# Kernel optimization log

Hardware: AMD Instinct MI355X
Metric: run time of the kernel (lower is better)

## Reference

```python
import jax, jax.numpy as jnp
import numpy as np
import math

B, L, F, R = 64, 16, 64, 1023


def setup_inputs() -> dict:
    key = jax.random.key(0)
    ks = jax.random.split(key, 12)

    def prob(k):
        p = jax.random.uniform(k, (B, L), dtype=jnp.float32) + 1e-3
        return p / p.sum(-1, keepdims=True)  # sparsemax-style simplex weights

    x = jax.random.normal(ks[0], (B, L, F, R), dtype=jnp.float32)
    car_w = prob(ks[1])
    cdr_w = prob(ks[2])
    cons1_w = prob(ks[3])
    cons2_w = prob(ks[4])
    root_filler = jax.random.normal(ks[5], (B, F), dtype=jnp.float32)
    s = 0.05
    D_l = jax.random.normal(ks[6], (R, R), dtype=jnp.float32) * s
    D_r = jax.random.normal(ks[7], (R, R), dtype=jnp.float32) * s
    E_l = jax.random.normal(ks[8], (R, R), dtype=jnp.float32) * s
    E_r = jax.random.normal(ks[9], (R, R), dtype=jnp.float32) * s
    root_role = jax.random.normal(ks[10], (R,), dtype=jnp.float32)
    return dict(x=x, car_w=car_w, cdr_w=cdr_w, cons1_w=cons1_w, cons2_w=cons2_w,
                root_filler=root_filler, D_l=D_l, D_r=D_r, E_l=E_l, E_r=E_r,
                root_role=root_role)


def _entropy(p):
    # torch.distributions.Categorical(p).entropy() / log(num_cats)
    return -(p * jnp.log(p + 1e-12)).sum(-1) / math.log(p.shape[-1])


def reference(x, car_w, cdr_w, cons1_w, cons2_w, root_filler, D_l, D_r, E_l, E_r, root_role):
    # --- CarNet (dense branch, empty_filler_initialization != 'random') ---
    car_arg = jnp.einsum('blfr,bl->bfr', x, car_w)          # weighted memory read
    car_out = jnp.einsum('bfr,tr->bft', car_arg, D_l)       # left-child extraction
    # --- CdrNet ---
    cdr_arg = jnp.einsum('blfr,bl->bfr', x, cdr_w)
    cdr_out = jnp.einsum('bfr,tr->bft', cdr_arg, D_r)       # right-child extraction
    # --- ConsNet ---
    c1 = jnp.einsum('blfr,bl->bfr', x, cons1_w)
    c2 = jnp.einsum('blfr,bl->bfr', x, cons2_w)
    cons_out = (jnp.einsum('bfr,tr->bft', c1, E_l)
                + jnp.einsum('bfr,tr->bft', c2, E_r)
                + root_filler[:, :, None] * root_role[None, None, :])
    ents = (_entropy(car_w), _entropy(cdr_w), _entropy(cons1_w), _entropy(cons2_w))
    maxes = (car_w.max(1), cdr_w.max(1), cons1_w.max(1), cons2_w.max(1))
    return (car_out, cdr_out, cons_out) + ents + maxes
```

## Files before the change

### kernel.cpp

```cpp
#include <hip/hip_runtime.h>
#include <hip/hip_bf16.h>
#include <hip/hip_fp8.h>
#include <stdint.h>

#define Rdim 1023
#define BFR  4190208

typedef float  f32x4  __attribute__((ext_vector_type(4)));
typedef float  f32x4u __attribute__((ext_vector_type(4), aligned(4)));

__device__ __forceinline__ void async16(const void* g, void* l) {
    __builtin_amdgcn_global_load_lds(
        (const __attribute__((address_space(1))) void*)g,
        (__attribute__((address_space(3))) void*)l, 16, 0, 0);
}

#define BAR()  do { __builtin_amdgcn_s_barrier(); __builtin_amdgcn_sched_barrier(0); } while(0)

__device__ __forceinline__ uint32_t f2fp8(float f) {
    __hip_fp8_e4m3 v(f);
    return (uint32_t)v.__x;
}
__device__ __forceinline__ uint32_t pack4(const float* a, float s) {
    return f2fp8(s*a[0]) | (f2fp8(s*a[1])<<8) | (f2fp8(s*a[2])<<16) | (f2fp8(s*a[3])<<24);
}

__global__ __launch_bounds__(256) void k_prep(
    const float* __restrict__ x,
    const float* __restrict__ w0, const float* __restrict__ w1,
    const float* __restrict__ w2, const float* __restrict__ w3,
    const float* __restrict__ Dl, const float* __restrict__ Dr,
    const float* __restrict__ El, const float* __restrict__ Er,
    uint8_t* __restrict__ args8, uint8_t* __restrict__ dpad8,
    float* __restrict__ out)
{
    const int blk = blockIdx.x;
    const int t   = threadIdx.x;

    if (blk < 1024) {
        const int id = blk*256 + t;
        const float* src; int n, c16, r0; size_t dst; int stride;
        if (id < 131072) {
            const int mat = id >> 16;
            src = mat ? Dr : Dl;
            const int rem = id & 65535;
            n = rem >> 6; c16 = rem & 63; r0 = c16*16; stride = 1024;
            dst = (mat ? 1048576u : 0u);
        } else {
            const int rem = id - 131072;
            n = rem >> 7; c16 = rem & 127;
            r0 = (c16 & 63)*16; stride = 2048;
            src = (c16 < 64) ? El : Er;
            dst = 2097152u;
        }
        const int pos = ((c16 >> 2) << 6) + (((c16 & 3) ^ ((n >> 1) & 3)) << 4);
        float v[16] = {};
        if (n < Rdim) {
            const float* sp = src + (size_t)n*Rdim + r0;
            if (r0 <= Rdim - 16) {
#pragma unroll
                for (int j = 0; j < 4; ++j) {
                    f32x4u u = *(const f32x4u*)(sp + j*4);
#pragma unroll
                    for (int q = 0; q < 4; ++q) v[j*4+q] = u[q];
                }
            } else {
#pragma unroll
                for (int j = 0; j < 3; ++j) {
                    f32x4u u = *(const f32x4u*)(sp + j*4);
#pragma unroll
                    for (int q = 0; q < 4; ++q) v[j*4+q] = u[q];
                }
                v[12] = sp[12]; v[13] = sp[13]; v[14] = sp[14];
            }
        }
        uint32_t w[4];
#pragma unroll
        for (int j = 0; j < 4; ++j) w[j] = pack4(v + j*4, 16.f);
        *(uint4*)(dpad8 + dst + (size_t)n*stride + pos) =
            make_uint4(w[0], w[1], w[2], w[3]);
    } else if (blk < 5120) {
        const int m = blk - 1024;
        const int b = m >> 6;
        float wr0[16], wr1[16], wr2[16], wr3[16];
#pragma unroll
        for (int l = 0; l < 16; ++l) {
            wr0[l] = w0[b*16 + l]; wr1[l] = w1[b*16 + l];
            wr2[l] = w2[b*16 + l]; wr3[l] = w3[b*16 + l];
        }
        const float* xb = x + ((size_t)(b*16)*64 + (m & 63)) * (size_t)Rdim;
        float a0[4] = {}, a1[4] = {}, a2[4] = {}, a3[4] = {};
        if (t < 255) {
#pragma unroll
            for (int l = 0; l < 16; ++l) {
                f32x4u v = *(const f32x4u*)(xb + (size_t)l*(64*(size_t)Rdim) + t*4);
#pragma unroll
                for (int j = 0; j < 4; ++j) {
                    a0[j] += wr0[l]*v[j]; a1[j] += wr1[l]*v[j];
                    a2[j] += wr2[l]*v[j]; a3[j] += wr3[l]*v[j];
                }
            }
        } else {
#pragma unroll
            for (int l = 0; l < 16; ++l) {
                const float* p = xb + (size_t)l*(64*(size_t)Rdim) + 1020;
#pragma unroll
                for (int j = 0; j < 3; ++j) {
                    float v = p[j];
                    a0[j] += wr0[l]*v; a1[j] += wr1[l]*v;
                    a2[j] += wr2[l]*v; a3[j] += wr3[l]*v;
                }
            }
        }
        const int r0  = t*4;
        const int S2  = (m >> 1) & 3;
        const int pos = ((r0 >> 6) << 6) + ((((r0 >> 4) & 3) ^ S2) << 4) + (r0 & 15);
        *(uint32_t*)(args8 +            (size_t)m*1024 + pos) = pack4(a0, 1.f);
        *(uint32_t*)(args8 + 4194304 +  (size_t)m*1024 + pos) = pack4(a1, 1.f);
        uint8_t* c12 = args8 + 8388608 + (size_t)m*2048;
        *(uint32_t*)(c12 + pos)        = pack4(a2, 1.f);
        *(uint32_t*)(c12 + 1024 + pos) = pack4(a3, 1.f);
    } else {
        const int k = t >> 6, b2 = t & 63;
        const float* w = (k==0) ? w0 : (k==1) ? w1 : (k==2) ? w2 : w3;
        float s = 0.f, mx = -1e30f;
#pragma unroll
        for (int l = 0; l < 16; ++l) {
            float p = w[b2*16 + l];
            s += p * logf(p + 1e-12f);
            mx = fmaxf(mx, p);
        }
        out[3*(size_t)BFR +       k*64 + b2] = -s / logf(16.f);
        out[3*(size_t)BFR + 256 + k*64 + b2] = mx;
    }
}

template<int BM, int NKT, int VM, bool CONS>
__device__ __forceinline__ void gemm_t(
    const uint8_t* __restrict__ Ab, const uint8_t* __restrict__ Bb,
    const float* __restrict__ rf, const float* __restrict__ rr,
    float* __restrict__ outp, char* lds, int mt, int nt)
{
    constexpr int AstB = CONS ? 2048 : 1024;
    constexpr int MI   = BM / 32;
    constexpr int ABUF = BM * 64;

    const int tid  = threadIdx.x;
    const int wave = tid >> 6, lane = tid & 63;
    const int wm   = wave >> 2, wn = wave & 3;
    const int lr   = lane & 15, lk = lane >> 4;
    const int sw   = (lr >> 1) & 3;
    const int cb0 = ((((lk >> 1)    ) ^ sw) << 4) + ((lk & 1) << 3);
    const int cb1 = (((2 + (lk >> 1)) ^ sw) << 4) + ((lk & 1) << 3);

    const uint8_t* AgT = Ab + (size_t)(mt*BM  + (tid>>2))*AstB + (tid&3)*16;
    const uint8_t* BgT = Bb + (size_t)(nt*256 + (tid>>2))*AstB + (tid&3)*16;

    f32x4 acc[MI][4] = {};
    long af[MI][2], bfr[4][2];

#define STG(bufidx, kt) do {                                                  \
    char* _a = lds + (bufidx)*ABUF + wave*1024;                               \
    char* _b = lds + 49152 + (bufidx)*16384 + wave*1024;                      \
    const size_t _ko = (size_t)(kt)*64;                                       \
    _Pragma("unroll") for (int i = 0; i < BM/128; ++i)                        \
        async16(AgT + (size_t)(i*128)*AstB + _ko, _a + i*8192);               \
    _Pragma("unroll") for (int i = 0; i < 2; ++i)                             \
        async16(BgT + (size_t)(i*128)*AstB + _ko, _b + i*8192);               \
} while(0)

    STG(0, 0); STG(1, 1);
    asm volatile("s_waitcnt vmcnt(%0)" :: "n"(VM) : "memory");
    BAR();

    int cb = 0;
    for (int kt = 0; kt < NKT; ++kt) {
        char* cA = lds + cb*ABUF;
        char* cB = lds + 49152 + cb*16384;
        int sb = cb + 2; if (sb >= 3) sb -= 3;
        const bool st = (kt + 2 < NKT);
#pragma unroll
        for (int mi = 0; mi < MI; ++mi) {
            const char* rp = cA + (wm*(BM/2) + mi*16 + lr)*64;
            af[mi][0] = *(const long*)(rp + cb0);
            af[mi][1] = *(const long*)(rp + cb1);
        }
#pragma unroll
        for (int j = 0; j < 4; ++j) {
            const char* rp = cB + (wn*64 + j*16 + lr)*64;
            bfr[j][0] = *(const long*)(rp + cb0);
            bfr[j][1] = *(const long*)(rp + cb1);
        }
        if (st) STG(sb, kt+2);
        __builtin_amdgcn_s_setprio(1);
#pragma unroll
        for (int ks = 0; ks < 2; ++ks)
#pragma unroll
        for (int mi = 0; mi < MI; ++mi)
#pragma unroll
        for (int j = 0; j < 4; ++j)
            acc[mi][j] = __builtin_amdgcn_mfma_f32_16x16x32_fp8_fp8(
                af[mi][ks], bfr[j][ks], acc[mi][j], 0, 0, 0);
        __builtin_amdgcn_s_setprio(0);
        if (st)                { asm volatile("s_waitcnt vmcnt(%0)" :: "n"(VM) : "memory"); }
        else if (kt == NKT-2)  { asm volatile("s_waitcnt vmcnt(0)" ::: "memory"); }
        BAR();
        cb = cb + 1; if (cb == 3) cb = 0;
    }
#undef STG

#pragma unroll
    for (int mi = 0; mi < MI; ++mi) {
        const int gm0 = mt*BM + wm*(BM/2) + mi*16 + lk*4;
#pragma unroll
        for (int j = 0; j < 4; ++j) {
            const int gn = nt*256 + wn*64 + j*16 + lr;
            if (gn < Rdim) {
                const float rv = CONS ? rr[gn] : 0.f;
#pragma unroll
                for (int q = 0; q < 4; ++q) {
                    float v = acc[mi][j][q] * 0.0625f;
                    if (CONS) v += rf[gm0 + q] * rv;
                    outp[(size_t)(gm0 + q)*Rdim + gn] = v;
                }
            }
        }
    }
}

__global__ __launch_bounds__(512, 1) void k_gemm(
    const uint8_t* __restrict__ args8, const uint8_t* __restrict__ dpad8,
    const float* __restrict__ root_filler, const float* __restrict__ root_role,
    float* __restrict__ out)
{
    __shared__ char lds[98304];
    const int bid = blockIdx.x;
    const int xcd = bid & 7, idx = bid >> 3;

    if (idx < 16) {
        const int tile = xcd*16 + idx;
        gemm_t<128, 32, 3, true >(args8 + 8388608, dpad8 + 2097152,
            root_filler, root_role, out + 2*(size_t)BFR, lds, tile >> 2, tile & 3);
    } else if (idx < 24) {
        const int tile = xcd*8 + idx - 16;
        gemm_t<256, 16, 4, false>(args8, dpad8,
            root_filler, root_role, out, lds, tile >> 2, tile & 3);
    } else {
        const int tile = xcd*8 + idx - 24;
        gemm_t<256, 16, 4, false>(args8 + 4194304, dpad8 + 1048576,
            root_filler, root_role, out + (size_t)BFR, lds, tile >> 2, tile & 3);
    }
}

extern "C" void kernel_launch(void* const* d_in, const int* in_sizes, int n_in,
                              void* d_out, int out_size, void* d_ws, size_t ws_size,
                              hipStream_t stream)
{
    const float* x           = (const float*)d_in[0];
    const float* car_w       = (const float*)d_in[1];
    const float* cdr_w       = (const float*)d_in[2];
    const float* cons1_w     = (const float*)d_in[3];
    const float* cons2_w     = (const float*)d_in[4];
    const float* root_filler = (const float*)d_in[5];
    const float* Dl          = (const float*)d_in[6];
    const float* Dr          = (const float*)d_in[7];
    const float* El          = (const float*)d_in[8];
    const float* Er          = (const float*)d_in[9];
    const float* root_role   = (const float*)d_in[10];
    float* out = (float*)d_out;

    uint8_t* args8 = (uint8_t*)d_ws;
    uint8_t* dpad8 = args8 + 16777216;

    k_prep<<<dim3(5121), dim3(256), 0, stream>>>(
        x, car_w, cdr_w, cons1_w, cons2_w, Dl, Dr, El, Er, args8, dpad8, out);
    k_gemm<<<dim3(256),  dim3(512), 0, stream>>>(
        args8, dpad8, root_filler, root_role, out);
}
```

Measured before the change: 102.7 us.

## Split cons GEMM K dimension into two uniform tiles and merge partials

The cons GEMM used to run as 128-row tiles with a K length of 2048. It is now split into two K=1024 halves, so every block in the fused GEMM launch runs an identical 256x256 tile with 16 K-steps, which balances per-block work across the 256 workgroups. The second half writes fp32 partials to a workspace buffer, and a new merge kernel adds them into the cons output. In exchange the change adds an extra kernel launch plus about 16 MB each of fp32 partial writes, reads and a read-modify-write of the cons output.

```diff
diff --git a/kernel.cpp b/kernel.cpp
--- a/kernel.cpp
+++ b/kernel.cpp
@@ -135,15 +135,14 @@
     }
 }
 
-template<int BM, int NKT, int VM, bool CONS>
+template<int AstB, int EPI>
 __device__ __forceinline__ void gemm_t(
     const uint8_t* __restrict__ Ab, const uint8_t* __restrict__ Bb,
     const float* __restrict__ rf, const float* __restrict__ rr,
     float* __restrict__ outp, char* lds, int mt, int nt)
 {
-    constexpr int AstB = CONS ? 2048 : 1024;
-    constexpr int MI   = BM / 32;
-    constexpr int ABUF = BM * 64;
+    constexpr int MI   = 8;
+    constexpr int ABUF = 16384;
 
     const int tid  = threadIdx.x;
     const int wave = tid >> 6, lane = tid & 63;
@@ -153,7 +152,7 @@
     const int cb0 = ((((lk >> 1)    ) ^ sw) << 4) + ((lk & 1) << 3);
     const int cb1 = (((2 + (lk >> 1)) ^ sw) << 4) + ((lk & 1) << 3);
 
-    const uint8_t* AgT = Ab + (size_t)(mt*BM  + (tid>>2))*AstB + (tid&3)*16;
+    const uint8_t* AgT = Ab + (size_t)(mt*256 + (tid>>2))*AstB + (tid&3)*16;
     const uint8_t* BgT = Bb + (size_t)(nt*256 + (tid>>2))*AstB + (tid&3)*16;
 
     f32x4 acc[MI][4] = {};
@@ -163,25 +162,25 @@
     char* _a = lds + (bufidx)*ABUF + wave*1024;                               \
     char* _b = lds + 49152 + (bufidx)*16384 + wave*1024;                      \
     const size_t _ko = (size_t)(kt)*64;                                       \
-    _Pragma("unroll") for (int i = 0; i < BM/128; ++i)                        \
+    _Pragma("unroll") for (int i = 0; i < 2; ++i)                             \
         async16(AgT + (size_t)(i*128)*AstB + _ko, _a + i*8192);               \
     _Pragma("unroll") for (int i = 0; i < 2; ++i)                             \
         async16(BgT + (size_t)(i*128)*AstB + _ko, _b + i*8192);               \
 } while(0)
 
     STG(0, 0); STG(1, 1);
-    asm volatile("s_waitcnt vmcnt(%0)" :: "n"(VM) : "memory");
+    asm volatile("s_waitcnt vmcnt(4)" ::: "memory");
     BAR();
 
     int cb = 0;
-    for (int kt = 0; kt < NKT; ++kt) {
+    for (int kt = 0; kt < 16; ++kt) {
         char* cA = lds + cb*ABUF;
         char* cB = lds + 49152 + cb*16384;
         int sb = cb + 2; if (sb >= 3) sb -= 3;
-        const bool st = (kt + 2 < NKT);
+        const bool st = (kt + 2 < 16);
 #pragma unroll
         for (int mi = 0; mi < MI; ++mi) {
-            const char* rp = cA + (wm*(BM/2) + mi*16 + lr)*64;
+            const char* rp = cA + (wm*128 + mi*16 + lr)*64;
             af[mi][0] = *(const long*)(rp + cb0);
             af[mi][1] = *(const long*)(rp + cb1);
         }
@@ -202,8 +201,8 @@
             acc[mi][j] = __builtin_amdgcn_mfma_f32_16x16x32_fp8_fp8(
                 af[mi][ks], bfr[j][ks], acc[mi][j], 0, 0, 0);
         __builtin_amdgcn_s_setprio(0);
-        if (st)                { asm volatile("s_waitcnt vmcnt(%0)" :: "n"(VM) : "memory"); }
-        else if (kt == NKT-2)  { asm volatile("s_waitcnt vmcnt(0)" ::: "memory"); }
+        if (st)           { asm volatile("s_waitcnt vmcnt(4)" ::: "memory"); }
+        else if (kt == 14){ asm volatile("s_waitcnt vmcnt(0)" ::: "memory"); }
         BAR();
         cb = cb + 1; if (cb == 3) cb = 0;
     }
@@ -211,16 +210,16 @@
 
 #pragma unroll
     for (int mi = 0; mi < MI; ++mi) {
-        const int gm0 = mt*BM + wm*(BM/2) + mi*16 + lk*4;
+        const int gm0 = mt*256 + wm*128 + mi*16 + lk*4;
 #pragma unroll
         for (int j = 0; j < 4; ++j) {
             const int gn = nt*256 + wn*64 + j*16 + lr;
             if (gn < Rdim) {
-                const float rv = CONS ? rr[gn] : 0.f;
+                const float rv = (EPI == 1) ? rr[gn] : 0.f;
 #pragma unroll
                 for (int q = 0; q < 4; ++q) {
                     float v = acc[mi][j][q] * 0.0625f;
-                    if (CONS) v += rf[gm0 + q] * rv;
+                    if (EPI == 1) v += rf[gm0 + q] * rv;
                     outp[(size_t)(gm0 + q)*Rdim + gn] = v;
                 }
             }
@@ -231,24 +230,43 @@
 __global__ __launch_bounds__(512, 1) void k_gemm(
     const uint8_t* __restrict__ args8, const uint8_t* __restrict__ dpad8,
     const float* __restrict__ root_filler, const float* __restrict__ root_role,
-    float* __restrict__ out)
+    float* __restrict__ out, float* __restrict__ P)
 {
     __shared__ char lds[98304];
     const int bid = blockIdx.x;
     const int xcd = bid & 7, idx = bid >> 3;
-
-    if (idx < 16) {
-        const int tile = xcd*16 + idx;
-        gemm_t<128, 32, 3, true >(args8 + 8388608, dpad8 + 2097152,
-            root_filler, root_role, out + 2*(size_t)BFR, lds, tile >> 2, tile & 3);
-    } else if (idx < 24) {
-        const int tile = xcd*8 + idx - 16;
-        gemm_t<256, 16, 4, false>(args8, dpad8,
-            root_filler, root_role, out, lds, tile >> 2, tile & 3);
-    } else {
-        const int tile = xcd*8 + idx - 24;
-        gemm_t<256, 16, 4, false>(args8 + 4194304, dpad8 + 1048576,
-            root_filler, root_role, out + (size_t)BFR, lds, tile >> 2, tile & 3);
+    const int job = idx >> 3;
+    const int tile = xcd*8 + (idx & 7);
+    const int mt = tile >> 2, nt = tile & 3;
+
+    if (job == 0)
+        gemm_t<1024, 0>(args8, dpad8,
+            root_filler, root_role, out, lds, mt, nt);
+    else if (job == 1)
+        gemm_t<1024, 0>(args8 + 4194304, dpad8 + 1048576,
+            root_filler, root_role, out + (size_t)BFR, lds, mt, nt);
+    else if (job == 2)
+        gemm_t<2048, 1>(args8 + 8388608, dpad8 + 2097152,
+            root_filler, root_role, out + 2*(size_t)BFR, lds, mt, nt);
+    else
+        gemm_t<2048, 0>(args8 + 8388608 + 1024, dpad8 + 2097152 + 1024,
+            root_filler, root_role, P, lds, mt, nt);
+}
+
+__global__ __launch_bounds__(256) void k_merge(
+    const float* __restrict__ P, float* __restrict__ out)
+{
+    const int i = blockIdx.x*256 + threadIdx.x;
+    float* o = out + 2*(size_t)BFR;
+#pragma unroll
+    for (int r = 0; r < 4; ++r) {
+        const int v = i + r*262144;
+        if (v < 1047552) {
+            f32x4 a = *(const f32x4*)(o + (size_t)v*4);
+            f32x4 b = *(const f32x4*)(P + (size_t)v*4);
+            a = a + b;
+            *(f32x4*)(o + (size_t)v*4) = a;
+        }
     }
 }
 
@@ -271,9 +289,11 @@
 
     uint8_t* args8 = (uint8_t*)d_ws;
     uint8_t* dpad8 = args8 + 16777216;
-
-    k_prep<<<dim3(5121), dim3(256), 0, stream>>>(
+    float*   P     = (float*)((char*)d_ws + 20971520);
+
+    k_prep <<<dim3(5121), dim3(256), 0, stream>>>(
         x, car_w, cdr_w, cons1_w, cons2_w, Dl, Dr, El, Er, args8, dpad8, out);
-    k_gemm<<<dim3(256),  dim3(512), 0, stream>>>(
-        args8, dpad8, root_filler, root_role, out);
-}
+    k_gemm <<<dim3(256),  dim3(512), 0, stream>>>(
+        args8, dpad8, root_filler, root_role, out, P);
+    k_merge<<<dim3(1024), dim3(256), 0, stream>>>(P, out);
+}
```

After: 112.1 us. 1.09x slower.

## Use 128-wide K tiles with 8-way swizzle for cons GEMM

Applied to the files above, without the earlier changes.

The cons GEMM (K=2048) now stages 128-byte K slices per iteration, taking 16 iterations instead of 32. The prep kernel writes its operands in a matching 8-way XOR swizzled layout so LDS reads stay conflict-free at the 128-byte row stride. This halves the number of barriers and pipeline steps in the cons tiles so they finish in line with the car/cdr tiles. In exchange, LDS grows to 144 KB, and register pressure from the 4x4 fragment arrays rises.

```diff
diff --git a/kernel.cpp b/kernel.cpp
--- a/kernel.cpp
+++ b/kernel.cpp
@@ -39,21 +39,23 @@
 
     if (blk < 1024) {
         const int id = blk*256 + t;
-        const float* src; int n, c16, r0; size_t dst; int stride;
+        const float* src; int n, c16, r0; size_t dst; int stride; bool consr;
         if (id < 131072) {
             const int mat = id >> 16;
             src = mat ? Dr : Dl;
             const int rem = id & 65535;
             n = rem >> 6; c16 = rem & 63; r0 = c16*16; stride = 1024;
-            dst = (mat ? 1048576u : 0u);
+            dst = (mat ? 1048576u : 0u); consr = false;
         } else {
             const int rem = id - 131072;
             n = rem >> 7; c16 = rem & 127;
             r0 = (c16 & 63)*16; stride = 2048;
             src = (c16 < 64) ? El : Er;
-            dst = 2097152u;
-        }
-        const int pos = ((c16 >> 2) << 6) + (((c16 & 3) ^ ((n >> 1) & 3)) << 4);
+            dst = 2097152u; consr = true;
+        }
+        const int pos = consr
+            ? ((c16 >> 3) << 7) + (((c16 & 7) ^ (n & 7)) << 4)
+            : ((c16 >> 2) << 6) + (((c16 & 3) ^ ((n >> 1) & 3)) << 4);
         float v[16] = {};
         if (n < Rdim) {
             const float* sp = src + (size_t)n*Rdim + r0;
@@ -112,14 +114,15 @@
                 }
             }
         }
-        const int r0  = t*4;
-        const int S2  = (m >> 1) & 3;
-        const int pos = ((r0 >> 6) << 6) + ((((r0 >> 4) & 3) ^ S2) << 4) + (r0 & 15);
-        *(uint32_t*)(args8 +            (size_t)m*1024 + pos) = pack4(a0, 1.f);
-        *(uint32_t*)(args8 + 4194304 +  (size_t)m*1024 + pos) = pack4(a1, 1.f);
+        const int r0 = t*4;
+        const int S2   = (m >> 1) & 3;
+        const int posO = ((r0 >> 6) << 6) + ((((r0 >> 4) & 3) ^ S2) << 4) + (r0 & 15);
+        const int posC = (r0 & ~127) + ((((r0 >> 4) & 7) ^ (m & 7)) << 4) + (r0 & 15);
+        *(uint32_t*)(args8 +            (size_t)m*1024 + posO) = pack4(a0, 1.f);
+        *(uint32_t*)(args8 + 4194304 +  (size_t)m*1024 + posO) = pack4(a1, 1.f);
         uint8_t* c12 = args8 + 8388608 + (size_t)m*2048;
-        *(uint32_t*)(c12 + pos)        = pack4(a2, 1.f);
-        *(uint32_t*)(c12 + 1024 + pos) = pack4(a3, 1.f);
+        *(uint32_t*)(c12 + posC)        = pack4(a2, 1.f);
+        *(uint32_t*)(c12 + 1024 + posC) = pack4(a3, 1.f);
     } else {
         const int k = t >> 6, b2 = t & 63;
         const float* w = (k==0) ? w0 : (k==1) ? w1 : (k==2) ? w2 : w3;
@@ -135,16 +138,11 @@
     }
 }
 
-template<int BM, int NKT, int VM, bool CONS>
-__device__ __forceinline__ void gemm_t(
+__device__ __forceinline__ void gemm_cc(
     const uint8_t* __restrict__ Ab, const uint8_t* __restrict__ Bb,
-    const float* __restrict__ rf, const float* __restrict__ rr,
     float* __restrict__ outp, char* lds, int mt, int nt)
 {
-    constexpr int AstB = CONS ? 2048 : 1024;
-    constexpr int MI   = BM / 32;
-    constexpr int ABUF = BM * 64;
-
+    constexpr int AstB = 1024;
     const int tid  = threadIdx.x;
     const int wave = tid >> 6, lane = tid & 63;
     const int wm   = wave >> 2, wn = wave & 3;
@@ -153,35 +151,35 @@
     const int cb0 = ((((lk >> 1)    ) ^ sw) << 4) + ((lk & 1) << 3);
     const int cb1 = (((2 + (lk >> 1)) ^ sw) << 4) + ((lk & 1) << 3);
 
-    const uint8_t* AgT = Ab + (size_t)(mt*BM  + (tid>>2))*AstB + (tid&3)*16;
+    const uint8_t* AgT = Ab + (size_t)(mt*256 + (tid>>2))*AstB + (tid&3)*16;
     const uint8_t* BgT = Bb + (size_t)(nt*256 + (tid>>2))*AstB + (tid&3)*16;
 
-    f32x4 acc[MI][4] = {};
-    long af[MI][2], bfr[4][2];
+    f32x4 acc[8][4] = {};
+    long af[8][2], bfr[4][2];
 
 #define STG(bufidx, kt) do {                                                  \
-    char* _a = lds + (bufidx)*ABUF + wave*1024;                               \
+    char* _a = lds + (bufidx)*16384 + wave*1024;                              \
     char* _b = lds + 49152 + (bufidx)*16384 + wave*1024;                      \
-    const size_t _ko = (size_t)(kt)*64;                                       \
-    _Pragma("unroll") for (int i = 0; i < BM/128; ++i)                        \
+    const size_t _ko = (size_t)(kt)*64;                                      \
+    _Pragma("unroll") for (int i = 0; i < 2; ++i)                             \
         async16(AgT + (size_t)(i*128)*AstB + _ko, _a + i*8192);               \
     _Pragma("unroll") for (int i = 0; i < 2; ++i)                             \
         async16(BgT + (size_t)(i*128)*AstB + _ko, _b + i*8192);               \
 } while(0)
 
     STG(0, 0); STG(1, 1);
-    asm volatile("s_waitcnt vmcnt(%0)" :: "n"(VM) : "memory");
+    asm volatile("s_waitcnt vmcnt(4)" ::: "memory");
     BAR();
 
     int cb = 0;
-    for (int kt = 0; kt < NKT; ++kt) {
-        char* cA = lds + cb*ABUF;
+    for (int kt = 0; kt < 16; ++kt) {
+        char* cA = lds + cb*16384;
         char* cB = lds + 49152 + cb*16384;
         int sb = cb + 2; if (sb >= 3) sb -= 3;
-        const bool st = (kt + 2 < NKT);
-#pragma unroll
-        for (int mi = 0; mi < MI; ++mi) {
-            const char* rp = cA + (wm*(BM/2) + mi*16 + lr)*64;
+        const bool st = (kt + 2 < 16);
+#pragma unroll
+        for (int mi = 0; mi < 8; ++mi) {
+            const char* rp = cA + (wm*128 + mi*16 + lr)*64;
             af[mi][0] = *(const long*)(rp + cb0);
             af[mi][1] = *(const long*)(rp + cb1);
         }
@@ -196,31 +194,117 @@
 #pragma unroll
         for (int ks = 0; ks < 2; ++ks)
 #pragma unroll
-        for (int mi = 0; mi < MI; ++mi)
+        for (int mi = 0; mi < 8; ++mi)
 #pragma unroll
         for (int j = 0; j < 4; ++j)
             acc[mi][j] = __builtin_amdgcn_mfma_f32_16x16x32_fp8_fp8(
                 af[mi][ks], bfr[j][ks], acc[mi][j], 0, 0, 0);
         __builtin_amdgcn_s_setprio(0);
-        if (st)                { asm volatile("s_waitcnt vmcnt(%0)" :: "n"(VM) : "memory"); }
-        else if (kt == NKT-2)  { asm volatile("s_waitcnt vmcnt(0)" ::: "memory"); }
+        if (st)           { asm volatile("s_waitcnt vmcnt(4)" ::: "memory"); }
+        else if (kt == 14){ asm volatile("s_waitcnt vmcnt(0)" ::: "memory"); }
         BAR();
         cb = cb + 1; if (cb == 3) cb = 0;
     }
 #undef STG
 
 #pragma unroll
-    for (int mi = 0; mi < MI; ++mi) {
-        const int gm0 = mt*BM + wm*(BM/2) + mi*16 + lk*4;
+    for (int mi = 0; mi < 8; ++mi) {
+        const int gm0 = mt*256 + wm*128 + mi*16 + lk*4;
 #pragma unroll
         for (int j = 0; j < 4; ++j) {
             const int gn = nt*256 + wn*64 + j*16 + lr;
             if (gn < Rdim) {
-                const float rv = CONS ? rr[gn] : 0.f;
+#pragma unroll
+                for (int q = 0; q < 4; ++q)
+                    outp[(size_t)(gm0 + q)*Rdim + gn] = acc[mi][j][q] * 0.0625f;
+            }
+        }
+    }
+}
+
+__device__ __forceinline__ void gemm_cons(
+    const uint8_t* __restrict__ Ab, const uint8_t* __restrict__ Bb,
+    const float* __restrict__ rf, const float* __restrict__ rr,
+    float* __restrict__ outp, char* lds, int mt, int nt)
+{
+    const int tid  = threadIdx.x;
+    const int wave = tid >> 6, lane = tid & 63;
+    const int wm   = wave >> 2, wn = wave & 3;
+    const int lr   = lane & 15, lk = lane >> 4;
+    int cbs[4];
+#pragma unroll
+    for (int ks = 0; ks < 4; ++ks)
+        cbs[ks] = (((ks*2 + (lk >> 1)) ^ (lr & 7)) << 4) + ((lk & 1) << 3);
+
+    const uint8_t* AgT = Ab + (size_t)(mt*128 + (tid>>3))*2048 + (tid&7)*16;
+    const uint8_t* BgT = Bb + (size_t)(nt*256 + (tid>>3))*2048 + (tid&7)*16;
+
+    f32x4 acc[4][4] = {};
+    long af[4][4], bfr[4][4];
+
+#define STGC(bufidx, kt) do {                                                 \
+    char* _a = lds + (bufidx)*16384 + wave*1024;                              \
+    char* _b = lds + 49152 + (bufidx)*32768 + wave*1024;                      \
+    const size_t _ko = (size_t)(kt)*128;                                      \
+    async16(AgT + _ko, _a);                                                   \
+    async16(AgT + (size_t)64*2048 + _ko, _a + 8192);                          \
+    _Pragma("unroll") for (int i = 0; i < 4; ++i)                             \
+        async16(BgT + (size_t)(i*64)*2048 + _ko, _b + i*8192);                \
+} while(0)
+
+    STGC(0, 0); STGC(1, 1);
+    asm volatile("s_waitcnt vmcnt(6)" ::: "memory");
+    BAR();
+
+    int cb = 0;
+    for (int kt = 0; kt < 16; ++kt) {
+        char* cA = lds + cb*16384;
+        char* cB = lds + 49152 + cb*32768;
+        int sb = cb + 2; if (sb >= 3) sb -= 3;
+        const bool st = (kt + 2 < 16);
+#pragma unroll
+        for (int mi = 0; mi < 4; ++mi) {
+            const char* rp = cA + (wm*64 + mi*16 + lr)*128;
+#pragma unroll
+            for (int ks = 0; ks < 4; ++ks)
+                af[mi][ks] = *(const long*)(rp + cbs[ks]);
+        }
+#pragma unroll
+        for (int j = 0; j < 4; ++j) {
+            const char* rp = cB + (wn*64 + j*16 + lr)*128;
+#pragma unroll
+            for (int ks = 0; ks < 4; ++ks)
+                bfr[j][ks] = *(const long*)(rp + cbs[ks]);
+        }
+        if (st) STGC(sb, kt+2);
+        __builtin_amdgcn_s_setprio(1);
+#pragma unroll
+        for (int ks = 0; ks < 4; ++ks)
+#pragma unroll
+        for (int mi = 0; mi < 4; ++mi)
+#pragma unroll
+        for (int j = 0; j < 4; ++j)
+            acc[mi][j] = __builtin_amdgcn_mfma_f32_16x16x32_fp8_fp8(
+                af[mi][ks], bfr[j][ks], acc[mi][j], 0, 0, 0);
+        __builtin_amdgcn_s_setprio(0);
+        if (st)           { asm volatile("s_waitcnt vmcnt(6)" ::: "memory"); }
+        else if (kt == 14){ asm volatile("s_waitcnt vmcnt(0)" ::: "memory"); }
+        BAR();
+        cb = cb + 1; if (cb == 3) cb = 0;
+    }
+#undef STGC
+
+#pragma unroll
+    for (int mi = 0; mi < 4; ++mi) {
+        const int gm0 = mt*128 + wm*64 + mi*16 + lk*4;
+#pragma unroll
+        for (int j = 0; j < 4; ++j) {
+            const int gn = nt*256 + wn*64 + j*16 + lr;
+            if (gn < Rdim) {
+                const float rv = rr[gn];
 #pragma unroll
                 for (int q = 0; q < 4; ++q) {
-                    float v = acc[mi][j][q] * 0.0625f;
-                    if (CONS) v += rf[gm0 + q] * rv;
+                    float v = acc[mi][j][q] * 0.0625f + rf[gm0 + q] * rv;
                     outp[(size_t)(gm0 + q)*Rdim + gn] = v;
                 }
             }
@@ -233,22 +317,21 @@
     const float* __restrict__ root_filler, const float* __restrict__ root_role,
     float* __restrict__ out)
 {
-    __shared__ char lds[98304];
+    __shared__ char lds[147456];
     const int bid = blockIdx.x;
     const int xcd = bid & 7, idx = bid >> 3;
 
     if (idx < 16) {
         const int tile = xcd*16 + idx;
-        gemm_t<128, 32, 3, true >(args8 + 8388608, dpad8 + 2097152,
+        gemm_cons(args8 + 8388608, dpad8 + 2097152,
             root_filler, root_role, out + 2*(size_t)BFR, lds, tile >> 2, tile & 3);
     } else if (idx < 24) {
         const int tile = xcd*8 + idx - 16;
-        gemm_t<256, 16, 4, false>(args8, dpad8,
-            root_filler, root_role, out, lds, tile >> 2, tile & 3);
+        gemm_cc(args8, dpad8, out, lds, tile >> 2, tile & 3);
     } else {
         const int tile = xcd*8 + idx - 24;
-        gemm_t<256, 16, 4, false>(args8 + 4194304, dpad8 + 1048576,
-            root_filler, root_role, out + (size_t)BFR, lds, tile >> 2, tile & 3);
+        gemm_cc(args8 + 4194304, dpad8 + 1048576,
+            out + (size_t)BFR, lds, tile >> 2, tile & 3);
     }
 }
 
```

After: 100.7 us (median of 2 runs). About the same (-1.9%).
